# Kernel optimization log

Measured on AMD Instinct MI355X. Metric: run time of the kernel, lower is better.

The kernel has to match this reference:

```python
import jax, jax.numpy as jnp
import numpy as np

H = 150  # hidden per direction

def _lstm_dir(x, w_ih, w_hh, b_ih, b_hh):
    # x: [B, T, D] -> hs: [B, T, H]; PyTorch gate order i,f,g,o
    B = x.shape[0]
    xg = jnp.einsum('btd,gd->btg', x, w_ih) + b_ih + b_hh  # precompute input projection [B,T,4H]
    def step(carry, xt):
        h, c = carry
        g = xt + h @ w_hh.T
        i, f, gg, o = jnp.split(g, 4, axis=-1)
        i, f, o = jax.nn.sigmoid(i), jax.nn.sigmoid(f), jax.nn.sigmoid(o)
        c = f * c + i * jnp.tanh(gg)
        h = o * jnp.tanh(c)
        return (h, c), h
    init = (jnp.zeros((B, H), x.dtype), jnp.zeros((B, H), x.dtype))
    _, hs = jax.lax.scan(step, init, jnp.swapaxes(xg, 0, 1))  # [T,B,H]
    return jnp.swapaxes(hs, 0, 1)

def _bilstm(x, w_ih_f, w_hh_f, b_ih_f, b_hh_f, w_ih_b, w_hh_b, b_ih_b, b_hh_b):
    fwd = _lstm_dir(x, w_ih_f, w_hh_f, b_ih_f, b_hh_f)
    bwd = jnp.flip(_lstm_dir(jnp.flip(x, axis=1), w_ih_b, w_hh_b, b_ih_b, b_hh_b), axis=1)
    return jnp.concatenate([fwd, bwd], axis=-1)  # [B, T, 2H]

def setup_inputs() -> dict:
    key = jax.random.key(0)
    ks = jax.random.split(key, 20)
    s = 0.05
    d = {
        'sentences': jax.random.normal(ks[0], (1024, 128, 343), jnp.float32),
        'w_ih_f1': jax.random.normal(ks[1], (600, 343)) * s,
        'w_hh_f1': jax.random.normal(ks[2], (600, 150)) * s,
        'b_ih_f1': jax.random.normal(ks[3], (600,)) * s,
        'b_hh_f1': jax.random.normal(ks[4], (600,)) * s,
        'w_ih_b1': jax.random.normal(ks[5], (600, 343)) * s,
        'w_hh_b1': jax.random.normal(ks[6], (600, 150)) * s,
        'b_ih_b1': jax.random.normal(ks[7], (600,)) * s,
        'b_hh_b1': jax.random.normal(ks[8], (600,)) * s,
        'w_ih_f2': jax.random.normal(ks[9], (600, 300)) * s,
        'w_hh_f2': jax.random.normal(ks[10], (600, 150)) * s,
        'b_ih_f2': jax.random.normal(ks[11], (600,)) * s,
        'b_hh_f2': jax.random.normal(ks[12], (600,)) * s,
        'w_ih_b2': jax.random.normal(ks[13], (600, 300)) * s,
        'w_hh_b2': jax.random.normal(ks[14], (600, 150)) * s,
        'b_ih_b2': jax.random.normal(ks[15], (600,)) * s,
        'b_hh_b2': jax.random.normal(ks[16], (600,)) * s,
        'w_out': jax.random.normal(ks[17], (7, 300)) * s,
        'b_out': jax.random.normal(ks[18], (7,)) * s,
    }
    return d

def reference(sentences, w_ih_f1, w_hh_f1, b_ih_f1, b_hh_f1, w_ih_b1, w_hh_b1, b_ih_b1, b_hh_b1,
              w_ih_f2, w_hh_f2, b_ih_f2, b_hh_f2, w_ih_b2, w_hh_b2, b_ih_b2, b_hh_b2, w_out, b_out):
    # Layer 1: per-sentence BiLSTM over words, batched instead of a python loop (dropout is eval-mode identity)
    word_out = _bilstm(sentences, w_ih_f1, w_hh_f1, b_ih_f1, b_hh_f1, w_ih_b1, w_hh_b1, b_ih_b1, b_hh_b1)  # [S,T,300]
    sent_emb = jnp.max(word_out, axis=1)  # max-pool over words -> [S,300]
    # Layer 2: BiLSTM over the sequence of sentence embeddings (batch of 1 paragraph)
    sent_out = _bilstm(sent_emb[None], w_ih_f2, w_hh_f2, b_ih_f2, b_hh_f2, w_ih_b2, w_hh_b2, b_ih_b2, b_hh_b2)[0]  # [S,300]
    log_probs = jax.nn.log_softmax(sent_out @ w_out.T + b_out, axis=-1)  # [S,7]
    return log_probs
```

## Files before the change

kernel.cpp:

```cpp
#include <hip/hip_runtime.h>
#include <hip/hip_bf16.h>
#include <hip/hip_fp16.h>

typedef short bf16x8 __attribute__((ext_vector_type(8)));
typedef float f32x4 __attribute__((ext_vector_type(4)));
typedef unsigned short u16x4 __attribute__((ext_vector_type(4)));
typedef unsigned int uint32;

#define MFMA_B16(a,b,c) __builtin_amdgcn_mfma_f32_16x16x32_bf16(a,b,c,0,0,0)

#define NS   1024
#define TLEN 128
#define DD   343
#define HH   150
#define GG   600
#define KX   352
#define XR   360
#define HR   168
#define KXP  44
#define NP   640
#define NG2  640

#define OFF_WXP  0u
#define OFF_WHP  901120u
#define OFF_B1   1310720u
#define OFF_W2B  1315840u
#define OFF_W2I  1725440u
#define OFF_SE   3184640u
#define OFF_XG2  4413440u
#define OFF_H2O  9656320u
#define OFF_XBF  10885120u
#define NEED_BF  103159808ull

#define PE0 450560
#define PE1 655360
#define PE2 656640
#define PE3 861440
#define PE4 1226240

__device__ __forceinline__ float rcp_fast(float x) { return __builtin_amdgcn_rcpf(x); }
__device__ __forceinline__ float sigm(float x) { return rcp_fast(1.f + __expf(-x)); }
__device__ __forceinline__ float tanh_fast(float x) { return 1.f - 2.f * rcp_fast(__expf(2.f * x) + 1.f); }

typedef __attribute__((address_space(1))) const void GASV;
typedef __attribute__((address_space(3))) void LASV;
__device__ __forceinline__ void gload_lds16(const void* g, void* l) {
  __builtin_amdgcn_global_load_lds((GASV*)g, (LASV*)l, 16, 0, 0);
}

__device__ __forceinline__ void bar_lds() {
  asm volatile("s_waitcnt lgkmcnt(0)" ::: "memory");
  __builtin_amdgcn_s_barrier();
  asm volatile("" ::: "memory");
}
__device__ __forceinline__ void bar_full() {
  asm volatile("s_waitcnt vmcnt(0) lgkmcnt(0)" ::: "memory");
  __builtin_amdgcn_s_barrier();
  asm volatile("" ::: "memory");
}

__device__ __forceinline__ unsigned short f2bu(float v) {
  __hip_bfloat16 b = __float2bfloat16(v);
  return __builtin_bit_cast(unsigned short, b);
}

__global__ __launch_bounds__(256) void prep_kernel(
    const float* __restrict__ wif1, const float* __restrict__ whf1,
    const float* __restrict__ bif1, const float* __restrict__ bhf1,
    const float* __restrict__ wib1, const float* __restrict__ whb1,
    const float* __restrict__ bib1, const float* __restrict__ bhb1,
    const float* __restrict__ wif2, const float* __restrict__ wib2,
    const float* __restrict__ whf2, const float* __restrict__ whb2,
    __hip_bfloat16* __restrict__ WXp, __hip_bfloat16* __restrict__ WHp,
    float* __restrict__ B1, __hip_bfloat16* __restrict__ W2B, float* __restrict__ W2I)
{
  int i = blockIdx.x * 256 + threadIdx.x;
  if (i < PE0) {
    int d = i / 225280; int r = i - d * 225280;
    int p = r / 5120;   int r2 = r - p * 5120;
    int n2 = r2 >> 3;   int jj = r2 & 7;
    int k = p * 8 + jj;
    int g = n2 / 160, j = n2 - g * 160;
    const float* w = d ? wib1 : wif1;
    float v = (j < HH && k < DD) ? w[(g * HH + j) * DD + k] : 0.f;
    WXp[i] = __float2bfloat16(v);
  } else if (i < PE1) {
    int ii = i - PE0;
    int d = ii / 102400; int r = ii - d * 102400;
    int p = r / 5120;    int r2 = r - p * 5120;
    int n2 = r2 >> 3;    int jj = r2 & 7;
    int k = p * 8 + jj;
    int g = n2 / 160, j = n2 - g * 160;
    const float* w = d ? whb1 : whf1;
    float v = (j < HH && k < HH) ? w[(g * HH + j) * HH + k] : 0.f;
    WHp[ii] = __float2bfloat16(v);
  } else if (i < PE2) {
    int ii = i - PE1;
    int d = ii / NP; int n2 = ii - d * NP;
    int g = n2 / 160, j = n2 - g * 160;
    float v = 0.f;
    if (j < HH) {
      int n = g * HH + j;
      v = d ? (bib1[n] + bhb1[n]) : (bif1[n] + bhf1[n]);
    }
    B1[ii] = v;
  } else if (i < PE3) {
    int ii = i - PE2;
    int d = ii / 102400; int r = ii - d * 102400;
    int n2 = r / 160;    int k = r - n2 * 160;
    int g = n2 / 160, j = n2 - g * 160;
    const float* w = d ? whb2 : whf2;
    float v = (j < HH && k < HH) ? w[(g * HH + j) * HH + k] : 0.f;
    W2B[ii] = __float2bfloat16(v);
  } else if (i < PE4) {
    int ii = i - PE3;
    int d = ii / 182400; int r = ii - d * 182400;
    int k = r / 608;     int n = r - k * 608;
    const float* w = d ? wib2 : wif2;
    float v = (n < GG) ? w[n * 300 + k] : 0.f;
    W2I[ii] = v;
  }
}

__global__ __launch_bounds__(256) void xcvt_kernel(
    const float* __restrict__ x, __hip_bfloat16* __restrict__ XBF)
{
  const int total4 = NS * TLEN * (KX / 4);
  for (int idx = blockIdx.x * 256 + threadIdx.x; idx < total4; idx += gridDim.x * 256) {
    int row = idx / 88;
    int c4 = (idx - row * 88) * 4;
    const float* src = x + (size_t)row * DD + c4;
    float v0 = 0.f, v1 = 0.f, v2 = 0.f, v3 = 0.f;
    if (c4 + 3 < DD) {
      v0 = __builtin_nontemporal_load(src);
      v1 = __builtin_nontemporal_load(src + 1);
      v2 = __builtin_nontemporal_load(src + 2);
      v3 = __builtin_nontemporal_load(src + 3);
    } else {
      if (c4 < DD)     v0 = src[0];
      if (c4 + 1 < DD) v1 = src[1];
      if (c4 + 2 < DD) v2 = src[2];
    }
    u16x4 o;
    o.x = f2bu(v0); o.y = f2bu(v1); o.z = f2bu(v2); o.w = f2bu(v3);
    u16x4* dst = (u16x4*)((unsigned short*)XBF + (size_t)row * KX + c4);
    __builtin_nontemporal_store(o, dst);
  }
}

#define XS_SZ   46080u
#define HS_OFF  (2u * XS_SZ)
#define L1_SMEM (HS_OFF + 5376u)

template<bool BF>
__device__ __forceinline__ void stage_x(char* xsd, const float* __restrict__ x,
                                        const __hip_bfloat16* __restrict__ XBF,
                                        int t0, int dir, int s0, int tid, int lane, int wv)
{
  if constexpr (BF) {
    #pragma unroll
    for (int i = 0; i < 7; ++i) {
      int rid = wv + i * 10;
      if (rid < 64 && lane < 44) {
        int p = rid >> 4, rr = rid & 15;
        int t = t0 + 2 * p + (rr >> 3);
        int s = s0 + (rr & 7);
        int tt = dir ? (127 - t) : t;
        const __hip_bfloat16* gp = XBF + ((size_t)s * TLEN + tt) * KX + lane * 8;
        gload_lds16((const void*)gp, (void*)(xsd + rid * 720));
      }
    }
  } else {
    for (int e = tid; e < 4 * 16 * XR; e += 640) {
      int row16 = e / XR;
      int col = e - row16 * XR;
      int p = row16 >> 4, rr = row16 & 15;
      int t = t0 + 2 * p + (rr >> 3);
      int s = s0 + (rr & 7);
      int tt = dir ? (127 - t) : t;
      float v = (col < DD) ? x[((size_t)s * TLEN + tt) * DD + col] : 0.f;
      ((__hip_bfloat16*)xsd)[e] = __float2bfloat16(v);
    }
  }
}

template<bool BF>
__global__ __launch_bounds__(640)
void lstm1_kernel(
    const float* __restrict__ x, const __hip_bfloat16* __restrict__ XBF,
    const __hip_bfloat16* __restrict__ WXp, const __hip_bfloat16* __restrict__ WHp,
    const float* __restrict__ B1, float* __restrict__ SE)
{
  extern __shared__ char smem[];
  char* xs0 = smem;
  char* xs1 = smem + XS_SZ;
  __hip_bfloat16* hs = (__hip_bfloat16*)(smem + HS_OFF);

  const int tid = threadIdx.x;
  const int lane = tid & 63;
  const int wv = tid >> 6;
  const int dir = blockIdx.x & 1;
  const int s0 = (blockIdx.x >> 1) * 8;
  const int c16 = lane & 15;
  const int kgrp = lane >> 4;
  const int j = wv * 16 + c16;

  for (int e = tid; e < 16 * HR; e += 640) hs[e] = __float2bfloat16(0.f);

  float bias[4];
  #pragma unroll
  for (int g4 = 0; g4 < 4; ++g4) {
    bias[g4] = B1[dir * NP + g4 * 160 + j];
    asm volatile("" : "+v"(bias[g4]));
  }

  const __hip_bfloat16* WXd = WXp + (size_t)dir * KXP * NP * 8;
  const __hip_bfloat16* WHd = WHp + (size_t)dir * 20 * NP * 8;

  bf16x8 whr[5][4];
  #pragma unroll
  for (int kh = 0; kh < 5; ++kh)
    #pragma unroll
    for (int g4 = 0; g4 < 4; ++g4) {
      whr[kh][g4] = *reinterpret_cast<const bf16x8*>(
          WHd + ((size_t)(kh * 4 + kgrp) * NP + g4 * 160 + j) * 8);
      asm volatile("" : "+v"(whr[kh][g4]));
    }

  float creg[4] = {0.f, 0.f, 0.f, 0.f};
  float mxr[4] = {-3e38f, -3e38f, -3e38f, -3e38f};

  stage_x<BF>(xs0, x, XBF, 0, dir, s0, tid, lane, wv);
  bar_full();

  for (int g = 0; g < 16; ++g) {
    char* xsc = (g & 1) ? xs1 : xs0;
    char* xsn = (g & 1) ? xs0 : xs1;
    const __hip_bfloat16* xsb = (const __hip_bfloat16*)xsc;

    f32x4 acc[4][4];
    #pragma unroll
    for (int p = 0; p < 4; ++p)
      #pragma unroll
      for (int g4 = 0; g4 < 4; ++g4) acc[p][g4] = (f32x4){0.f, 0.f, 0.f, 0.f};

    for (int kk = 0; kk < 11; ++kk) {
      bf16x8 a[4], b[4];
      #pragma unroll
      for (int p = 0; p < 4; ++p)
        a[p] = *reinterpret_cast<const bf16x8*>(xsb + (p * 16 + c16) * XR + kk * 32 + kgrp * 8);
      #pragma unroll
      for (int g4 = 0; g4 < 4; ++g4)
        b[g4] = *reinterpret_cast<const bf16x8*>(
            WXd + ((size_t)(kk * 4 + kgrp) * NP + g4 * 160 + j) * 8);
      #pragma unroll
      for (int p = 0; p < 4; ++p)
        #pragma unroll
        for (int g4 = 0; g4 < 4; ++g4)
          acc[p][g4] = MFMA_B16(a[p], b[g4], acc[p][g4]);
    }

    if (g < 15)
      stage_x<BF>(xsn, x, XBF, (g + 1) * 8, dir, s0, tid, lane, wv);

    #pragma unroll
    for (int p = 0; p < 4; ++p) {
      #pragma unroll
      for (int kh = 0; kh < 5; ++kh) {
        bf16x8 ah = *reinterpret_cast<const bf16x8*>(hs + c16 * HR + kh * 32 + kgrp * 8);
        #pragma unroll
        for (int g4 = 0; g4 < 4; ++g4)
          acc[p][g4] = MFMA_B16(ah, whr[kh][g4], acc[p][g4]);
      }
      {
        const bool act = (kgrp < 2);
        #pragma unroll
        for (int r = 0; r < 4; ++r) {
          float iv = sigm(acc[p][0][r] + bias[0]);
          float fv = sigm(acc[p][1][r] + bias[1]);
          float gv = tanh_fast(acc[p][2][r] + bias[2]);
          float ov = sigm(acc[p][3][r] + bias[3]);
          float cin = __shfl_xor(creg[r], 32);
          float cn = fv * cin + iv * gv;
          float h = ov * tanh_fast(cn);
          creg[r] = act ? cn : creg[r];
          mxr[r] = act ? fmaxf(mxr[r], h) : mxr[r];
          if (act) hs[(8 + kgrp * 4 + r) * HR + j] = __float2bfloat16(h);
        }
      }
      bar_lds();
      #pragma unroll
      for (int kh = 0; kh < 5; ++kh) {
        bf16x8 ah = *reinterpret_cast<const bf16x8*>(hs + c16 * HR + kh * 32 + kgrp * 8);
        #pragma unroll
        for (int g4 = 0; g4 < 4; ++g4)
          acc[p][g4] = MFMA_B16(ah, whr[kh][g4], acc[p][g4]);
      }
      {
        const bool act = (kgrp >= 2);
        #pragma unroll
        for (int r = 0; r < 4; ++r) {
          float iv = sigm(acc[p][0][r] + bias[0]);
          float fv = sigm(acc[p][1][r] + bias[1]);
          float gv = tanh_fast(acc[p][2][r] + bias[2]);
          float ov = sigm(acc[p][3][r] + bias[3]);
          float cin = __shfl_xor(creg[r], 32);
          float cn = fv * cin + iv * gv;
          float h = ov * tanh_fast(cn);
          creg[r] = act ? cn : creg[r];
          mxr[r] = act ? fmaxf(mxr[r], h) : mxr[r];
          if (act) {
            int s = (kgrp - 2) * 4 + r;
            hs[s * HR + j] = __float2bfloat16(h);
            hs[(8 + s) * HR + j] = __float2bfloat16(0.f);
          }
        }
      }
      if (p == 3) bar_full(); else bar_lds();
    }
  }

  #pragma unroll
  for (int r = 0; r < 4; ++r) {
    float m = fmaxf(mxr[r], __shfl_xor(mxr[r], 32));
    if (kgrp < 2 && j < HH)
      SE[(size_t)(s0 + kgrp * 4 + r) * 300 + dir * HH + j] = m;
  }
}

__global__ __launch_bounds__(256, 1) void xg2_kernel(
    const float* __restrict__ SE, const float* __restrict__ W2I,
    const float* __restrict__ bif2, const float* __restrict__ bhf2,
    const float* __restrict__ bib2, const float* __restrict__ bhb2,
    float* __restrict__ XG2)
{
  __shared__ float se[32 * 304];
  const int d = blockIdx.x >> 5, st = blockIdx.x & 31, sb = st * 32;
  const int tid = threadIdx.x;
  for (int e = tid; e < 32 * 300; e += 256) {
    int si = e / 300, k = e - si * 300;
    se[si * 304 + k] = SE[(size_t)(sb + si) * 300 + k];
  }
  __syncthreads();
  for (int pass = 0; pass < 3; ++pass) {
    int n = pass * 256 + tid;
    if (n < GG) {
      int n2 = (n / 150) * 160 + (n % 150);
      float bias = d ? (bib2[n] + bhb2[n]) : (bif2[n] + bhf2[n]);
      float acc[32];
      #pragma unroll
      for (int si = 0; si < 32; ++si) acc[si] = bias;
      const float* wcol = W2I + (size_t)d * 300 * 608 + n;
      for (int k = 0; k < 300; ++k) {
        float wvv = wcol[(size_t)k * 608];
        #pragma unroll
        for (int si = 0; si < 32; ++si) acc[si] += wvv * se[si * 304 + k];
      }
      #pragma unroll
      for (int si = 0; si < 32; ++si)
        XG2[((size_t)d * NS + sb + si) * NG2 + n2] = acc[si];
    }
  }
  for (int e = tid; e < 32 * 40; e += 256) {
    int si = e / 40, q = e - si * 40;
    int g = q / 10, jp = 150 + (q - g * 10);
    XG2[((size_t)d * NS + sb + si) * NG2 + g * 160 + jp] = 0.f;
  }
}

__global__ __launch_bounds__(640) void lstm2_kernel(
    const __hip_bfloat16* __restrict__ W2B, const float* __restrict__ XG2,
    float* __restrict__ H2O)
{
  const int dir = blockIdx.x;
  const int tid = threadIdx.x;
  const int lane = tid & 63;
  const int wv = tid >> 6;
  const int c16 = lane & 15;
  const int kg = lane >> 4;
  const int j = wv * 16 + c16;
  __shared__ __align__(16) __hip_bfloat16 hbuf[2][160];

  const f32x4 ZERO4 = {0.f, 0.f, 0.f, 0.f};

  const __hip_bfloat16* Wd = W2B + (size_t)dir * NP * 160;
  bf16x8 wf[5][4];
  #pragma unroll
  for (int kt = 0; kt < 5; ++kt)
    #pragma unroll
    for (int g4 = 0; g4 < 4; ++g4) {
      wf[kt][g4] = *reinterpret_cast<const bf16x8*>(
          Wd + (size_t)(g4 * 160 + j) * 160 + kt * 32 + kg * 8);
      asm volatile("" : "+v"(wf[kt][g4]));
    }

  if (tid < 160) hbuf[0][tid] = __float2bfloat16(0.f);
  __syncthreads();

  float creg = 0.f;
  const float* xg = XG2 + (size_t)dir * NS * NG2;
  float xv[4];
  {
    int ss0 = dir ? 1023 : 0;
    #pragma unroll
    for (int g4 = 0; g4 < 4; ++g4) xv[g4] = xg[(size_t)ss0 * NG2 + g4 * 160 + j];
  }

  for (int step = 0; step < 1024; ++step) {
    const int ss = dir ? (1023 - step) : step;
    float xn[4] = {0.f, 0.f, 0.f, 0.f};
    if (step < 1023) {
      int ss2 = dir ? (1022 - step) : (step + 1);
      #pragma unroll
      for (int g4 = 0; g4 < 4; ++g4) xn[g4] = xg[(size_t)ss2 * NG2 + g4 * 160 + j];
    }
    const int cur = step & 1;
    bf16x8 hf[5];
    #pragma unroll
    for (int kt = 0; kt < 5; ++kt)
      hf[kt] = *reinterpret_cast<const bf16x8*>(&hbuf[cur][kt * 32 + kg * 8]);
    f32x4 aA[4], aB[4];
    #pragma unroll
    for (int g4 = 0; g4 < 4; ++g4) {
      aA[g4] = MFMA_B16(hf[0], wf[0][g4], ZERO4);
      aB[g4] = MFMA_B16(hf[1], wf[1][g4], ZERO4);
    }
    #pragma unroll
    for (int g4 = 0; g4 < 4; ++g4) {
      aA[g4] = MFMA_B16(hf[2], wf[2][g4], aA[g4]);
      aB[g4] = MFMA_B16(hf[3], wf[3][g4], aB[g4]);
      aA[g4] = MFMA_B16(hf[4], wf[4][g4], aA[g4]);
    }
    float iv = sigm(aA[0][0] + aB[0][0] + xv[0]);
    float fv = sigm(aA[1][0] + aB[1][0] + xv[1]);
    float gv = tanh_fast(aA[2][0] + aB[2][0] + xv[2]);
    float ov = sigm(aA[3][0] + aB[3][0] + xv[3]);
    creg = fv * creg + iv * gv;
    float nh = ov * tanh_fast(creg);
    if (kg == 0) {
      hbuf[cur ^ 1][j] = __float2bfloat16(nh);
      if (j < HH) H2O[(size_t)ss * 300 + dir * HH + j] = nh;
    }
    bar_lds();
    #pragma unroll
    for (int g4 = 0; g4 < 4; ++g4) xv[g4] = xn[g4];
  }
}

__global__ __launch_bounds__(256, 1) void head_kernel(
    const float* __restrict__ H2O, const float* __restrict__ w_out,
    const float* __restrict__ b_out, float* __restrict__ out)
{
  int s = blockIdx.x * 256 + threadIdx.x;
  if (s >= NS) return;
  float acc[7];
  #pragma unroll
  for (int c = 0; c < 7; ++c) acc[c] = b_out[c];
  const float* hrow = H2O + (size_t)s * 300;
  for (int k = 0; k < 300; ++k) {
    float hv = hrow[k];
    #pragma unroll
    for (int c = 0; c < 7; ++c) acc[c] += hv * w_out[c * 300 + k];
  }
  float m = acc[0];
  #pragma unroll
  for (int c = 1; c < 7; ++c) m = fmaxf(m, acc[c]);
  float sum = 0.f;
  #pragma unroll
  for (int c = 0; c < 7; ++c) sum += __expf(acc[c] - m);
  float lse = m + __logf(sum);
  #pragma unroll
  for (int c = 0; c < 7; ++c) out[s * 7 + c] = acc[c] - lse;
}

extern "C" void kernel_launch(void* const* d_in, const int* in_sizes, int n_in,
                              void* d_out, int out_size, void* d_ws, size_t ws_size,
                              hipStream_t stream) {
  const float* x      = (const float*)d_in[0];
  const float* wif1   = (const float*)d_in[1];
  const float* whf1   = (const float*)d_in[2];
  const float* bif1   = (const float*)d_in[3];
  const float* bhf1   = (const float*)d_in[4];
  const float* wib1   = (const float*)d_in[5];
  const float* whb1   = (const float*)d_in[6];
  const float* bib1   = (const float*)d_in[7];
  const float* bhb1   = (const float*)d_in[8];
  const float* wif2   = (const float*)d_in[9];
  const float* whf2   = (const float*)d_in[10];
  const float* bif2   = (const float*)d_in[11];
  const float* bhf2   = (const float*)d_in[12];
  const float* wib2   = (const float*)d_in[13];
  const float* whb2   = (const float*)d_in[14];
  const float* bib2   = (const float*)d_in[15];
  const float* bhb2   = (const float*)d_in[16];
  const float* w_out  = (const float*)d_in[17];
  const float* b_out  = (const float*)d_in[18];

  char* ws = (char*)d_ws;
  __hip_bfloat16* WXp = (__hip_bfloat16*)(ws + OFF_WXP);
  __hip_bfloat16* WHp = (__hip_bfloat16*)(ws + OFF_WHP);
  float*    B1  = (float*)(ws + OFF_B1);
  __hip_bfloat16* W2B = (__hip_bfloat16*)(ws + OFF_W2B);
  float*    W2I = (float*)(ws + OFF_W2I);
  float*    SE  = (float*)(ws + OFF_SE);
  float*    XG2 = (float*)(ws + OFF_XG2);
  float*    H2O = (float*)(ws + OFF_H2O);
  __hip_bfloat16* XBF = (__hip_bfloat16*)(ws + OFF_XBF);

  const bool useBF = (ws_size >= NEED_BF);

  prep_kernel<<<(PE4 + 255) / 256, 256, 0, stream>>>(
      wif1, whf1, bif1, bhf1, wib1, whb1, bib1, bhb1,
      wif2, wib2, whf2, whb2, WXp, WHp, B1, W2B, W2I);

  if (useBF)
    xcvt_kernel<<<4096, 256, 0, stream>>>(x, XBF);

  (void)hipFuncSetAttribute((const void*)(lstm1_kernel<true>),
                            hipFuncAttributeMaxDynamicSharedMemorySize, L1_SMEM);
  (void)hipFuncSetAttribute((const void*)(lstm1_kernel<false>),
                            hipFuncAttributeMaxDynamicSharedMemorySize, L1_SMEM);

  if (useBF)
    lstm1_kernel<true><<<256, 640, L1_SMEM, stream>>>(x, XBF, WXp, WHp, B1, SE);
  else
    lstm1_kernel<false><<<256, 640, L1_SMEM, stream>>>(x, XBF, WXp, WHp, B1, SE);

  xg2_kernel<<<64, 256, 0, stream>>>(SE, W2I, bif2, bhf2, bib2, bhb2, XG2);

  lstm2_kernel<<<2, 640, 0, stream>>>(W2B, XG2, H2O);

  head_kernel<<<4, 256, 0, stream>>>(H2O, w_out, b_out, (float*)d_out);
}
```

Measured before the change: 1.604 ms.

## Stage x tiles through registers and break MFMA dependency chains in layer-2 recurrence

Replaces the direct global-to-LDS loads for the next x tile with nontemporal loads into registers that are issued before the recurrent h-step loop and written to LDS just before the final barrier. This lets the global load latency overlap the four recurrent sub-steps and removes the vmcnt wait that the direct-to-LDS path put on every barrier. In the layer-2 sequential kernel, each of the five K-chunk MFMAs now starts from zero and the partial sums are added in scalar code, which shortens the serial MFMA accumulation chain per step. The cost is more VGPRs for the staging buffer and extra VALU adds.

After: 2.066 ms. 28.8% more time.

```diff
diff --git a/kernel.cpp b/kernel.cpp
--- a/kernel.cpp
+++ b/kernel.cpp
@@ -5,6 +5,7 @@
 typedef short bf16x8 __attribute__((ext_vector_type(8)));
 typedef float f32x4 __attribute__((ext_vector_type(4)));
 typedef unsigned short u16x4 __attribute__((ext_vector_type(4)));
+typedef unsigned short u16x8 __attribute__((ext_vector_type(8)));
 typedef unsigned int uint32;
 
 #define MFMA_B16(a,b,c) __builtin_amdgcn_mfma_f32_16x16x32_bf16(a,b,c,0,0,0)
@@ -20,6 +21,7 @@
 #define KXP  44
 #define NP   640
 #define NG2  640
+#define NCHUNK 2816
 
 #define OFF_WXP  0u
 #define OFF_WHP  901120u
@@ -41,12 +43,6 @@
 __device__ __forceinline__ float rcp_fast(float x) { return __builtin_amdgcn_rcpf(x); }
 __device__ __forceinline__ float sigm(float x) { return rcp_fast(1.f + __expf(-x)); }
 __device__ __forceinline__ float tanh_fast(float x) { return 1.f - 2.f * rcp_fast(__expf(2.f * x) + 1.f); }
-
-typedef __attribute__((address_space(1))) const void GASV;
-typedef __attribute__((address_space(3))) void LASV;
-__device__ __forceinline__ void gload_lds16(const void* g, void* l) {
-  __builtin_amdgcn_global_load_lds((GASV*)g, (LASV*)l, 16, 0, 0);
-}
 
 __device__ __forceinline__ void bar_lds() {
   asm volatile("s_waitcnt lgkmcnt(0)" ::: "memory");
@@ -152,34 +148,39 @@
 #define HS_OFF  (2u * XS_SZ)
 #define L1_SMEM (HS_OFF + 5376u)
 
-template<bool BF>
-__device__ __forceinline__ void stage_x(char* xsd, const float* __restrict__ x,
-                                        const __hip_bfloat16* __restrict__ XBF,
-                                        int t0, int dir, int s0, int tid, int lane, int wv)
-{
-  if constexpr (BF) {
-    #pragma unroll
-    for (int i = 0; i < 7; ++i) {
-      int rid = wv + i * 10;
-      if (rid < 64 && lane < 44) {
-        int p = rid >> 4, rr = rid & 15;
-        int t = t0 + 2 * p + (rr >> 3);
-        int s = s0 + (rr & 7);
-        int tt = dir ? (127 - t) : t;
-        const __hip_bfloat16* gp = XBF + ((size_t)s * TLEN + tt) * KX + lane * 8;
-        gload_lds16((const void*)gp, (void*)(xsd + rid * 720));
-      }
-    }
-  } else {
-    for (int e = tid; e < 4 * 16 * XR; e += 640) {
-      int row16 = e / XR;
-      int col = e - row16 * XR;
-      int p = row16 >> 4, rr = row16 & 15;
-      int t = t0 + 2 * p + (rr >> 3);
-      int s = s0 + (rr & 7);
-      int tt = dir ? (127 - t) : t;
-      float v = (col < DD) ? x[((size_t)s * TLEN + tt) * DD + col] : 0.f;
-      ((__hip_bfloat16*)xsd)[e] = __float2bfloat16(v);
+__device__ __forceinline__ void chunk_addr(int e, int t0, int dir, int s0,
+                                           int& row16, int& col16, size_t& goff)
+{
+  row16 = e / 44; col16 = e - row16 * 44;
+  int p = row16 >> 4, rr = row16 & 15;
+  int t = t0 + 2 * p + (rr >> 3);
+  int s = s0 + (rr & 7);
+  int tt = dir ? (127 - t) : t;
+  goff = ((size_t)s * TLEN + tt) * KX + col16 * 8;
+}
+
+__device__ __forceinline__ void stage_load(u16x8* xreg, const __hip_bfloat16* __restrict__ XBF,
+                                           int t0, int dir, int s0, int tid)
+{
+  #pragma unroll
+  for (int i = 0; i < 5; ++i) {
+    int e = tid + i * 640;
+    if (e < NCHUNK) {
+      int row16, col16; size_t goff;
+      chunk_addr(e, t0, dir, s0, row16, col16, goff);
+      xreg[i] = __builtin_nontemporal_load((const u16x8*)(XBF + goff));
+    }
+  }
+}
+
+__device__ __forceinline__ void stage_write(char* xsd, const u16x8* xreg, int tid)
+{
+  #pragma unroll
+  for (int i = 0; i < 5; ++i) {
+    int e = tid + i * 640;
+    if (e < NCHUNK) {
+      int row16 = e / 44, col16 = e - row16 * 44;
+      *(u16x8*)(xsd + row16 * 720 + col16 * 16) = xreg[i];
     }
   }
 }
@@ -230,7 +231,22 @@
   float creg[4] = {0.f, 0.f, 0.f, 0.f};
   float mxr[4] = {-3e38f, -3e38f, -3e38f, -3e38f};
 
-  stage_x<BF>(xs0, x, XBF, 0, dir, s0, tid, lane, wv);
+  u16x8 xreg[5];
+  if constexpr (BF) {
+    stage_load(xreg, XBF, 0, dir, s0, tid);
+    asm volatile("s_waitcnt vmcnt(0)" ::: "memory");
+    stage_write(xs0, xreg, tid);
+  } else {
+    for (int e = tid; e < 4 * 16 * XR; e += 640) {
+      int row16 = e / XR, col = e - row16 * XR;
+      int p = row16 >> 4, rr = row16 & 15;
+      int t = 2 * p + (rr >> 3);
+      int s = s0 + (rr & 7);
+      int tt = dir ? (127 - t) : t;
+      float v = (col < DD) ? x[((size_t)s * TLEN + tt) * DD + col] : 0.f;
+      ((__hip_bfloat16*)xs0)[e] = __float2bfloat16(v);
+    }
+  }
   bar_full();
 
   for (int g = 0; g < 16; ++g) {
@@ -260,8 +276,21 @@
           acc[p][g4] = MFMA_B16(a[p], b[g4], acc[p][g4]);
     }
 
-    if (g < 15)
-      stage_x<BF>(xsn, x, XBF, (g + 1) * 8, dir, s0, tid, lane, wv);
+    if (g < 15) {
+      if constexpr (BF) {
+        stage_load(xreg, XBF, (g + 1) * 8, dir, s0, tid);
+      } else {
+        for (int e = tid; e < 4 * 16 * XR; e += 640) {
+          int row16 = e / XR, col = e - row16 * XR;
+          int p = row16 >> 4, rr = row16 & 15;
+          int t = (g + 1) * 8 + 2 * p + (rr >> 3);
+          int s = s0 + (rr & 7);
+          int tt = dir ? (127 - t) : t;
+          float v = (col < DD) ? x[((size_t)s * TLEN + tt) * DD + col] : 0.f;
+          ((__hip_bfloat16*)xsn)[e] = __float2bfloat16(v);
+        }
+      }
+    }
 
     #pragma unroll
     for (int p = 0; p < 4; ++p) {
@@ -316,7 +345,17 @@
           }
         }
       }
-      if (p == 3) bar_full(); else bar_lds();
+      if (p == 3) {
+        if constexpr (BF) {
+          if (g < 15) {
+            asm volatile("s_waitcnt vmcnt(0)" ::: "memory");
+            stage_write(xsn, xreg, tid);
+          }
+        }
+        bar_full();
+      } else {
+        bar_lds();
+      }
     }
   }
 
@@ -419,22 +458,20 @@
     #pragma unroll
     for (int kt = 0; kt < 5; ++kt)
       hf[kt] = *reinterpret_cast<const bf16x8*>(&hbuf[cur][kt * 32 + kg * 8]);
-    f32x4 aA[4], aB[4];
+    float y[4];
     #pragma unroll
     for (int g4 = 0; g4 < 4; ++g4) {
-      aA[g4] = MFMA_B16(hf[0], wf[0][g4], ZERO4);
-      aB[g4] = MFMA_B16(hf[1], wf[1][g4], ZERO4);
-    }
-    #pragma unroll
-    for (int g4 = 0; g4 < 4; ++g4) {
-      aA[g4] = MFMA_B16(hf[2], wf[2][g4], aA[g4]);
-      aB[g4] = MFMA_B16(hf[3], wf[3][g4], aB[g4]);
-      aA[g4] = MFMA_B16(hf[4], wf[4][g4], aA[g4]);
-    }
-    float iv = sigm(aA[0][0] + aB[0][0] + xv[0]);
-    float fv = sigm(aA[1][0] + aB[1][0] + xv[1]);
-    float gv = tanh_fast(aA[2][0] + aB[2][0] + xv[2]);
-    float ov = sigm(aA[3][0] + aB[3][0] + xv[3]);
+      f32x4 c0 = MFMA_B16(hf[0], wf[0][g4], ZERO4);
+      f32x4 c1 = MFMA_B16(hf[1], wf[1][g4], ZERO4);
+      f32x4 c2 = MFMA_B16(hf[2], wf[2][g4], ZERO4);
+      f32x4 c3 = MFMA_B16(hf[3], wf[3][g4], ZERO4);
+      f32x4 c4 = MFMA_B16(hf[4], wf[4][g4], ZERO4);
+      y[g4] = ((c0[0] + c1[0]) + (c2[0] + c3[0])) + c4[0];
+    }
+    float iv = sigm(y[0] + xv[0]);
+    float fv = sigm(y[1] + xv[1]);
+    float gv = tanh_fast(y[2] + xv[2]);
+    float ov = sigm(y[3] + xv[3]);
     creg = fv * creg + iv * gv;
     float nh = ov * tanh_fast(creg);
     if (kg == 0) {
```

## Split layer-1 LSTM into separate input-projection GEMM and recurrence kernels

Applied to the files above, without the earlier changes.

Adds a path, taken when the workspace is large enough, where a standalone bf16 MFMA GEMM precomputes the layer-1 input gates for all timesteps into a large fp32 buffer. A lighter recurrent kernel then only does the hidden-state matmul and gate math, interleaving two time parities per block. The layer-2 recurrence loop is also unrolled by two, with fixed hbuf indices and the x-gate prefetch batched per pair of steps. The split writes and re-reads roughly 670 MB of gate values through global memory, trading that traffic against shorter recurrent critical paths.

Measured after the change: 1.610 ms. Within noise of the previous version (+0.4%).

```diff
diff --git a/kernel.cpp b/kernel.cpp
--- a/kernel.cpp
+++ b/kernel.cpp
@@ -31,6 +31,8 @@
 #define OFF_H2O  9656320u
 #define OFF_XBF  10885120u
 #define NEED_BF  103159808ull
+#define OFF_XG1  103159808ull
+#define NEED_SPLIT 774248448ull
 
 #define PE0 450560
 #define PE1 655360
@@ -148,6 +150,212 @@
   }
 }
 
+#define GA_SMEM (128u * 720u)
+
+__global__ __launch_bounds__(512) void xg1_gemm(
+    const __hip_bfloat16* __restrict__ XBF, const __hip_bfloat16* __restrict__ WXp,
+    const float* __restrict__ B1, float* __restrict__ XG1)
+{
+  extern __shared__ char smem[];
+  __hip_bfloat16* xsA = (__hip_bfloat16*)smem;
+
+  const int bid = blockIdx.x;
+  const int mt = bid / 10;
+  const int ntile = bid - mt * 10;
+  const int dir = ntile / 5;
+  const int nb = (ntile - dir * 5) * 128;
+  const int m0 = mt * 128;
+
+  const int tid = threadIdx.x;
+  const int lane = tid & 63;
+  const int wv = tid >> 6;
+  const int wr = wv >> 2;
+  const int wc = wv & 3;
+  const int arow = lane & 15;
+  const int kgrp = lane >> 4;
+
+  #pragma unroll
+  for (int i = 0; i < 16; ++i) {
+    int rid = wv * 16 + i;
+    if (lane < 44) {
+      const __hip_bfloat16* gp = XBF + (size_t)(m0 + rid) * KX + lane * 8;
+      gload_lds16((const void*)gp, (void*)(smem + rid * 720));
+    }
+  }
+  bar_full();
+
+  const __hip_bfloat16* WXd = WXp + (size_t)dir * KXP * NP * 8;
+
+  f32x4 acc[4][2];
+  #pragma unroll
+  for (int mi = 0; mi < 4; ++mi)
+    #pragma unroll
+    for (int ni = 0; ni < 2; ++ni) acc[mi][ni] = (f32x4){0.f, 0.f, 0.f, 0.f};
+
+  for (int kk = 0; kk < 11; ++kk) {
+    bf16x8 a[4], b[2];
+    #pragma unroll
+    for (int mi = 0; mi < 4; ++mi)
+      a[mi] = *reinterpret_cast<const bf16x8*>(
+          xsA + (wr * 64 + mi * 16 + arow) * XR + kk * 32 + kgrp * 8);
+    #pragma unroll
+    for (int ni = 0; ni < 2; ++ni)
+      b[ni] = *reinterpret_cast<const bf16x8*>(
+          WXd + ((size_t)(kk * 4 + kgrp) * NP + nb + wc * 32 + ni * 16 + arow) * 8);
+    #pragma unroll
+    for (int mi = 0; mi < 4; ++mi)
+      #pragma unroll
+      for (int ni = 0; ni < 2; ++ni)
+        acc[mi][ni] = MFMA_B16(a[mi], b[ni], acc[mi][ni]);
+  }
+
+  float bias[2];
+  #pragma unroll
+  for (int ni = 0; ni < 2; ++ni)
+    bias[ni] = B1[dir * NP + nb + wc * 32 + ni * 16 + arow];
+
+  float* outd = XG1 + (size_t)dir * NS * TLEN * NG2;
+  #pragma unroll
+  for (int mi = 0; mi < 4; ++mi) {
+    #pragma unroll
+    for (int r = 0; r < 4; ++r) {
+      int m = m0 + wr * 64 + mi * 16 + kgrp * 4 + r;
+      int s = m >> 7, t = m & 127;
+      float* row = outd + ((size_t)s * TLEN + t) * NG2;
+      #pragma unroll
+      for (int ni = 0; ni < 2; ++ni)
+        row[nb + wc * 32 + ni * 16 + arow] = acc[mi][ni][r] + bias[ni];
+    }
+  }
+}
+
+__global__ __launch_bounds__(640) void lstm1_rec(
+    const float* __restrict__ XG1, const __hip_bfloat16* __restrict__ WHp,
+    float* __restrict__ SE)
+{
+  __shared__ __hip_bfloat16 hs[16 * HR];
+
+  const int tid = threadIdx.x;
+  const int lane = tid & 63;
+  const int wv = tid >> 6;
+  const int dir = blockIdx.x & 1;
+  const int s0 = (blockIdx.x >> 1) * 8;
+  const int c16 = lane & 15;
+  const int kgrp = lane >> 4;
+  const int j = wv * 16 + c16;
+
+  for (int e = tid; e < 16 * HR; e += 640) hs[e] = __float2bfloat16(0.f);
+
+  const __hip_bfloat16* WHd = WHp + (size_t)dir * 20 * NP * 8;
+  bf16x8 whr[5][4];
+  #pragma unroll
+  for (int kh = 0; kh < 5; ++kh)
+    #pragma unroll
+    for (int g4 = 0; g4 < 4; ++g4) {
+      whr[kh][g4] = *reinterpret_cast<const bf16x8*>(
+          WHd + ((size_t)(kh * 4 + kgrp) * NP + g4 * 160 + j) * 8);
+      asm volatile("" : "+v"(whr[kh][g4]));
+    }
+
+  float creg[4] = {0.f, 0.f, 0.f, 0.f};
+  float mxr[4] = {-3e38f, -3e38f, -3e38f, -3e38f};
+
+  const float* xgd = XG1 + (size_t)dir * NS * TLEN * NG2;
+  const int sentb = s0 + (kgrp & 1) * 4;
+  const int par = kgrp >> 1;
+
+  float xq[16], xqN[16];
+  #pragma unroll
+  for (int g4 = 0; g4 < 4; ++g4)
+    #pragma unroll
+    for (int r = 0; r < 4; ++r) {
+      int tl = par;
+      int tt = dir ? (127 - tl) : tl;
+      xq[g4 * 4 + r] = xgd[((size_t)(sentb + r) * TLEN + tt) * NG2 + g4 * 160 + j];
+    }
+  __syncthreads();
+
+  for (int p = 0; p < 64; ++p) {
+    f32x4 acc[4];
+    #pragma unroll
+    for (int g4 = 0; g4 < 4; ++g4) {
+      acc[g4][0] = xq[g4 * 4 + 0]; acc[g4][1] = xq[g4 * 4 + 1];
+      acc[g4][2] = xq[g4 * 4 + 2]; acc[g4][3] = xq[g4 * 4 + 3];
+    }
+    if (p < 63) {
+      #pragma unroll
+      for (int g4 = 0; g4 < 4; ++g4)
+        #pragma unroll
+        for (int r = 0; r < 4; ++r) {
+          int tl = 2 * (p + 1) + par;
+          int tt = dir ? (127 - tl) : tl;
+          xqN[g4 * 4 + r] = xgd[((size_t)(sentb + r) * TLEN + tt) * NG2 + g4 * 160 + j];
+        }
+    }
+    #pragma unroll
+    for (int kh = 0; kh < 5; ++kh) {
+      bf16x8 ah = *reinterpret_cast<const bf16x8*>(hs + c16 * HR + kh * 32 + kgrp * 8);
+      #pragma unroll
+      for (int g4 = 0; g4 < 4; ++g4)
+        acc[g4] = MFMA_B16(ah, whr[kh][g4], acc[g4]);
+    }
+    {
+      const bool act = (kgrp < 2);
+      #pragma unroll
+      for (int r = 0; r < 4; ++r) {
+        float iv = sigm(acc[0][r]);
+        float fv = sigm(acc[1][r]);
+        float gv = tanh_fast(acc[2][r]);
+        float ov = sigm(acc[3][r]);
+        float cin = __shfl_xor(creg[r], 32);
+        float cn = fv * cin + iv * gv;
+        float h = ov * tanh_fast(cn);
+        creg[r] = act ? cn : creg[r];
+        mxr[r] = act ? fmaxf(mxr[r], h) : mxr[r];
+        if (act) hs[(8 + kgrp * 4 + r) * HR + j] = __float2bfloat16(h);
+      }
+    }
+    bar_lds();
+    #pragma unroll
+    for (int kh = 0; kh < 5; ++kh) {
+      bf16x8 ah = *reinterpret_cast<const bf16x8*>(hs + c16 * HR + kh * 32 + kgrp * 8);
+      #pragma unroll
+      for (int g4 = 0; g4 < 4; ++g4)
+        acc[g4] = MFMA_B16(ah, whr[kh][g4], acc[g4]);
+    }
+    {
+      const bool act = (kgrp >= 2);
+      #pragma unroll
+      for (int r = 0; r < 4; ++r) {
+        float iv = sigm(acc[0][r]);
+        float fv = sigm(acc[1][r]);
+        float gv = tanh_fast(acc[2][r]);
+        float ov = sigm(acc[3][r]);
+        float cin = __shfl_xor(creg[r], 32);
+        float cn = fv * cin + iv * gv;
+        float h = ov * tanh_fast(cn);
+        creg[r] = act ? cn : creg[r];
+        mxr[r] = act ? fmaxf(mxr[r], h) : mxr[r];
+        if (act) {
+          int s = (kgrp - 2) * 4 + r;
+          hs[s * HR + j] = __float2bfloat16(h);
+          hs[(8 + s) * HR + j] = __float2bfloat16(0.f);
+        }
+      }
+    }
+    bar_lds();
+    #pragma unroll
+    for (int q = 0; q < 16; ++q) xq[q] = xqN[q];
+  }
+
+  #pragma unroll
+  for (int r = 0; r < 4; ++r) {
+    float m = fmaxf(mxr[r], __shfl_xor(mxr[r], 32));
+    if (kgrp < 2 && j < HH)
+      SE[(size_t)(s0 + kgrp * 4 + r) * 300 + dir * HH + j] = m;
+  }
+}
+
 #define XS_SZ   46080u
 #define HS_OFF  (2u * XS_SZ)
 #define L1_SMEM (HS_OFF + 5376u)
@@ -399,51 +607,64 @@
 
   float creg = 0.f;
   const float* xg = XG2 + (size_t)dir * NS * NG2;
-  float xv[4];
-  {
-    int ss0 = dir ? 1023 : 0;
-    #pragma unroll
-    for (int g4 = 0; g4 < 4; ++g4) xv[g4] = xg[(size_t)ss0 * NG2 + g4 * 160 + j];
-  }
-
-  for (int step = 0; step < 1024; ++step) {
-    const int ss = dir ? (1023 - step) : step;
-    float xn[4] = {0.f, 0.f, 0.f, 0.f};
-    if (step < 1023) {
-      int ss2 = dir ? (1022 - step) : (step + 1);
-      #pragma unroll
-      for (int g4 = 0; g4 < 4; ++g4) xn[g4] = xg[(size_t)ss2 * NG2 + g4 * 160 + j];
-    }
-    const int cur = step & 1;
-    bf16x8 hf[5];
-    #pragma unroll
-    for (int kt = 0; kt < 5; ++kt)
-      hf[kt] = *reinterpret_cast<const bf16x8*>(&hbuf[cur][kt * 32 + kg * 8]);
-    f32x4 aA[4], aB[4];
+
+  float xqC[8], xqN[8];
+  #pragma unroll
+  for (int q = 0; q < 2; ++q)
     #pragma unroll
     for (int g4 = 0; g4 < 4; ++g4) {
-      aA[g4] = MFMA_B16(hf[0], wf[0][g4], ZERO4);
-      aB[g4] = MFMA_B16(hf[1], wf[1][g4], ZERO4);
-    }
-    #pragma unroll
-    for (int g4 = 0; g4 < 4; ++g4) {
-      aA[g4] = MFMA_B16(hf[2], wf[2][g4], aA[g4]);
-      aB[g4] = MFMA_B16(hf[3], wf[3][g4], aB[g4]);
-      aA[g4] = MFMA_B16(hf[4], wf[4][g4], aA[g4]);
-    }
-    float iv = sigm(aA[0][0] + aB[0][0] + xv[0]);
-    float fv = sigm(aA[1][0] + aB[1][0] + xv[1]);
-    float gv = tanh_fast(aA[2][0] + aB[2][0] + xv[2]);
-    float ov = sigm(aA[3][0] + aB[3][0] + xv[3]);
-    creg = fv * creg + iv * gv;
-    float nh = ov * tanh_fast(creg);
-    if (kg == 0) {
-      hbuf[cur ^ 1][j] = __float2bfloat16(nh);
-      if (j < HH) H2O[(size_t)ss * 300 + dir * HH + j] = nh;
-    }
-    bar_lds();
-    #pragma unroll
-    for (int g4 = 0; g4 < 4; ++g4) xv[g4] = xn[g4];
+      int sl = q;
+      int ss2 = dir ? (1023 - sl) : sl;
+      xqC[q * 4 + g4] = xg[(size_t)ss2 * NG2 + g4 * 160 + j];
+    }
+
+  for (int grp = 0; grp < 512; ++grp) {
+    #pragma unroll
+    for (int q = 0; q < 2; ++q)
+      #pragma unroll
+      for (int g4 = 0; g4 < 4; ++g4) {
+        int sl = grp * 2 + 2 + q;
+        if (sl < 1024) {
+          int ss2 = dir ? (1023 - sl) : sl;
+          xqN[q * 4 + g4] = xg[(size_t)ss2 * NG2 + g4 * 160 + j];
+        } else {
+          xqN[q * 4 + g4] = 0.f;
+        }
+      }
+    #pragma unroll
+    for (int q = 0; q < 2; ++q) {
+      const int step = grp * 2 + q;
+      const int ss = dir ? (1023 - step) : step;
+      bf16x8 hf[5];
+      #pragma unroll
+      for (int kt = 0; kt < 5; ++kt)
+        hf[kt] = *reinterpret_cast<const bf16x8*>(&hbuf[q][kt * 32 + kg * 8]);
+      f32x4 aA[4], aB[4];
+      #pragma unroll
+      for (int g4 = 0; g4 < 4; ++g4) {
+        aA[g4] = MFMA_B16(hf[0], wf[0][g4], ZERO4);
+        aB[g4] = MFMA_B16(hf[1], wf[1][g4], ZERO4);
+      }
+      #pragma unroll
+      for (int g4 = 0; g4 < 4; ++g4) {
+        aA[g4] = MFMA_B16(hf[2], wf[2][g4], aA[g4]);
+        aB[g4] = MFMA_B16(hf[3], wf[3][g4], aB[g4]);
+        aA[g4] = MFMA_B16(hf[4], wf[4][g4], aA[g4]);
+      }
+      float iv = sigm(aA[0][0] + aB[0][0] + xqC[q * 4 + 0]);
+      float fv = sigm(aA[1][0] + aB[1][0] + xqC[q * 4 + 1]);
+      float gv = tanh_fast(aA[2][0] + aB[2][0] + xqC[q * 4 + 2]);
+      float ov = sigm(aA[3][0] + aB[3][0] + xqC[q * 4 + 3]);
+      creg = fv * creg + iv * gv;
+      float nh = ov * tanh_fast(creg);
+      if (kg == 0) {
+        hbuf[q ^ 1][j] = __float2bfloat16(nh);
+        if (j < HH) H2O[(size_t)ss * 300 + dir * HH + j] = nh;
+      }
+      bar_lds();
+    }
+    #pragma unroll
+    for (int q = 0; q < 8; ++q) xqC[q] = xqN[q];
   }
 }
 
@@ -506,8 +727,10 @@
   float*    XG2 = (float*)(ws + OFF_XG2);
   float*    H2O = (float*)(ws + OFF_H2O);
   __hip_bfloat16* XBF = (__hip_bfloat16*)(ws + OFF_XBF);
+  float*    XG1 = (float*)(ws + OFF_XG1);
 
   const bool useBF = (ws_size >= NEED_BF);
+  const bool useSPLIT = (ws_size >= NEED_SPLIT);
 
   prep_kernel<<<(PE4 + 255) / 256, 256, 0, stream>>>(
       wif1, whf1, bif1, bhf1, wib1, whb1, bib1, bhb1,
@@ -516,15 +739,21 @@
   if (useBF)
     xcvt_kernel<<<4096, 256, 0, stream>>>(x, XBF);
 
-  (void)hipFuncSetAttribute((const void*)(lstm1_kernel<true>),
-                            hipFuncAttributeMaxDynamicSharedMemorySize, L1_SMEM);
-  (void)hipFuncSetAttribute((const void*)(lstm1_kernel<false>),
-                            hipFuncAttributeMaxDynamicSharedMemorySize, L1_SMEM);
-
-  if (useBF)
-    lstm1_kernel<true><<<256, 640, L1_SMEM, stream>>>(x, XBF, WXp, WHp, B1, SE);
-  else
-    lstm1_kernel<false><<<256, 640, L1_SMEM, stream>>>(x, XBF, WXp, WHp, B1, SE);
+  if (useSPLIT) {
+    (void)hipFuncSetAttribute((const void*)xg1_gemm,
+                              hipFuncAttributeMaxDynamicSharedMemorySize, GA_SMEM);
+    xg1_gemm<<<10240, 512, GA_SMEM, stream>>>(XBF, WXp, B1, XG1);
+    lstm1_rec<<<256, 640, 0, stream>>>(XG1, WHp, SE);
+  } else {
+    (void)hipFuncSetAttribute((const void*)(lstm1_kernel<true>),
+                              hipFuncAttributeMaxDynamicSharedMemorySize, L1_SMEM);
+    (void)hipFuncSetAttribute((const void*)(lstm1_kernel<false>),
+                              hipFuncAttributeMaxDynamicSharedMemorySize, L1_SMEM);
+    if (useBF)
+      lstm1_kernel<true><<<256, 640, L1_SMEM, stream>>>(x, XBF, WXp, WHp, B1, SE);
+    else
+      lstm1_kernel<false><<<256, 640, L1_SMEM, stream>>>(x, XBF, WXp, WHp, B1, SE);
+  }
 
   xg2_kernel<<<64, 256, 0, stream>>>(SE, W2I, bif2, bhf2, bib2, bhb2, XG2);
 
```
